# Performance work log

Measured on AMD Instinct MI355X. Metric: run time of the kernel, lower is better.

## Reference

```python
import jax, jax.numpy as jnp
import numpy as np

CODEBOOK_SIZE = 8192
DIM = 64
B, N = 4, 4096


def setup_inputs() -> dict:
    key = jax.random.key(0)
    k1, k2 = jax.random.split(key)
    x = jax.random.normal(k1, (B, N, DIM), dtype=jnp.float32)
    node_mask = jnp.ones((B, N), dtype=jnp.float32)
    embed = jax.random.normal(k2, (CODEBOOK_SIZE, DIM), dtype=jnp.float32)
    return {"x": x, "node_mask": node_mask, "embed": embed}


def reference(x, node_mask, embed):
    # x: [B, N, D]; embed: [K, D]; node_mask: [B, N]
    b, n, d = x.shape
    k = embed.shape[0]
    flatten = x.reshape(-1, d)  # [B*N, D]
    dist = -(
        jnp.sum(flatten * flatten, axis=1, keepdims=True)
        - 2.0 * (flatten @ embed.T)
        + jnp.sum(embed * embed, axis=1)[None, :]
    )
    embed_ind = jnp.argmax(dist, axis=-1)  # [B*N] nearest-code assignment
    quantize = embed[embed_ind].reshape(b, n, d)  # codebook gather
    # masked one-hot stats (embed_onehot * node_mask), via segment_sum
    mask_flat = node_mask.reshape(-1)
    counts = jax.ops.segment_sum(mask_flat, embed_ind, num_segments=k)  # [K]
    avg_probs = counts / jnp.asarray(flatten.shape[0], dtype=x.dtype)
    perplexity = jnp.exp(-jnp.sum(avg_probs * jnp.log(avg_probs + 1e-10)))
    return quantize, embed_ind.reshape(b, n), perplexity
```

## Files before the change

### kernel.cpp

```cpp
#include <hip/hip_runtime.h>

typedef __attribute__((ext_vector_type(8))) short short8;
typedef __attribute__((ext_vector_type(4))) float f32x4;

#define ROWS 16384
#define DIM 64
#define NCODES 8192
#define MARGIN 0.008f
#define KT_FB 256

#define WS_BEST   0
#define WS_COUNTS 131072
#define WS_ENH    163840
#define WS_ESWZ   196608
#define WS_NEED   2293760

__device__ __forceinline__ unsigned long long pack_score(float s, int idx) {
  unsigned u = __float_as_uint(s);
  u ^= (unsigned)((int)u >> 31) | 0x80000000u;
  return ((unsigned long long)u << 32) | (unsigned)(0xFFFF - idx);
}
__device__ __forceinline__ unsigned short bf16hi(float f) {
  unsigned u = __float_as_uint(f);
  return (unsigned short)((u + 0x7FFFu + ((u >> 16) & 1u)) >> 16);
}

__global__ void vq_enorm(const float* __restrict__ embed, float* __restrict__ enh) {
  int k = blockIdx.x * 256 + threadIdx.x;
  const float4* e4 = (const float4*)(embed + (size_t)k * DIM);
  float a = 0.f, b = 0.f, c = 0.f, d = 0.f;
#pragma unroll
  for (int i = 0; i < DIM / 4; ++i) {
    float4 v = e4[i];
    a = fmaf(v.x, v.x, a); b = fmaf(v.y, v.y, b);
    c = fmaf(v.z, v.z, c); d = fmaf(v.w, v.w, d);
  }
  enh[k] = 0.5f * ((a + b) + (c + d));
}

__global__ void vq_prep_e(const float* __restrict__ embed, short* __restrict__ eswz) {
  int u = blockIdx.x * 256 + threadIdx.x;
  int l = u & 63, kc = (u >> 6) & 1, ct = u >> 7;
  int code = ct * 16 + (l & 15);
  int kb = kc * 32 + (l >> 4) * 8;
  const float* er = embed + (size_t)code * DIM + kb;
  short8 h8, l8;
#pragma unroll
  for (int j = 0; j < 8; ++j) {
    float v = er[j];
    unsigned short h = bf16hi(v);
    float r = v - __uint_as_float((unsigned)h << 16);
    h8[j] = (short)h;
    l8[j] = (short)bf16hi(r);
  }
  short8* dst = (short8*)eswz;
  size_t frag = (size_t)(ct * 2 + kc) * 2;
  dst[(frag + 0) * 64 + l] = h8;
  dst[(frag + 1) * 64 + l] = l8;
}

__global__ __launch_bounds__(256, 2) void vq_screen(
    const float* __restrict__ x, const float* __restrict__ embed,
    const short* __restrict__ eswz, const float* __restrict__ enh,
    unsigned long long* __restrict__ best) {
  const int l = threadIdx.x & 63, wid = threadIdx.x >> 6;
  const int cl = l & 15, grp = l >> 4;
  const int row0 = blockIdx.x * 256 + wid * 64;
  const int ct0 = blockIdx.y * 64;

  short8 ahi[4][2], alo[4][2];
#pragma unroll
  for (int s = 0; s < 4; ++s) {
    const float* xr = x + (size_t)(row0 + s * 16 + cl) * DIM;
#pragma unroll
    for (int kc = 0; kc < 2; ++kc) {
      const int kb = kc * 32 + grp * 8;
#pragma unroll
      for (int j = 0; j < 8; ++j) {
        float v = xr[kb + j];
        unsigned short h = bf16hi(v);
        float r = v - __uint_as_float((unsigned)h << 16);
        ahi[s][kc][j] = (short)h;
        alo[s][kc][j] = (short)bf16hi(r);
      }
    }
  }

  const short8* eb = (const short8*)eswz;
  float bsc[4][4];
  int bidx[4][4];
#pragma unroll
  for (int s = 0; s < 4; ++s)
#pragma unroll
    for (int j = 0; j < 4; ++j) { bsc[s][j] = -3.4e38f; bidx[s][j] = 0; }

  short8 bh0, bl0, bh1, bl1;
  float eh;
  {
    size_t f0 = (size_t)(ct0 * 2 + 0) * 128, f1 = (size_t)(ct0 * 2 + 1) * 128;
    bh0 = eb[f0 + l]; bl0 = eb[f0 + 64 + l];
    bh1 = eb[f1 + l]; bl1 = eb[f1 + 64 + l];
    eh = enh[ct0 * 16 + cl];
  }

  for (int ct = ct0; ct < ct0 + 64; ++ct) {
    int ctn = (ct + 1 < ct0 + 64) ? ct + 1 : ct;
    size_t fn0 = (size_t)(ctn * 2 + 0) * 128, fn1 = (size_t)(ctn * 2 + 1) * 128;
    short8 nh0 = eb[fn0 + l], nl0 = eb[fn0 + 64 + l];
    short8 nh1 = eb[fn1 + l], nl1 = eb[fn1 + 64 + l];
    float ehx = enh[ctn * 16 + cl];

    f32x4 z = {0.f, 0.f, 0.f, 0.f};
    f32x4 acc0 = z, acc1 = z, acc2 = z, acc3 = z;
    acc0 = __builtin_amdgcn_mfma_f32_16x16x32_bf16(ahi[0][0], bh0, acc0, 0, 0, 0);
    acc1 = __builtin_amdgcn_mfma_f32_16x16x32_bf16(ahi[1][0], bh0, acc1, 0, 0, 0);
    acc2 = __builtin_amdgcn_mfma_f32_16x16x32_bf16(ahi[2][0], bh0, acc2, 0, 0, 0);
    acc3 = __builtin_amdgcn_mfma_f32_16x16x32_bf16(ahi[3][0], bh0, acc3, 0, 0, 0);
    acc0 = __builtin_amdgcn_mfma_f32_16x16x32_bf16(alo[0][0], bh0, acc0, 0, 0, 0);
    acc1 = __builtin_amdgcn_mfma_f32_16x16x32_bf16(alo[1][0], bh0, acc1, 0, 0, 0);
    acc2 = __builtin_amdgcn_mfma_f32_16x16x32_bf16(alo[2][0], bh0, acc2, 0, 0, 0);
    acc3 = __builtin_amdgcn_mfma_f32_16x16x32_bf16(alo[3][0], bh0, acc3, 0, 0, 0);
    acc0 = __builtin_amdgcn_mfma_f32_16x16x32_bf16(ahi[0][0], bl0, acc0, 0, 0, 0);
    acc1 = __builtin_amdgcn_mfma_f32_16x16x32_bf16(ahi[1][0], bl0, acc1, 0, 0, 0);
    acc2 = __builtin_amdgcn_mfma_f32_16x16x32_bf16(ahi[2][0], bl0, acc2, 0, 0, 0);
    acc3 = __builtin_amdgcn_mfma_f32_16x16x32_bf16(ahi[3][0], bl0, acc3, 0, 0, 0);
    acc0 = __builtin_amdgcn_mfma_f32_16x16x32_bf16(ahi[0][1], bh1, acc0, 0, 0, 0);
    acc1 = __builtin_amdgcn_mfma_f32_16x16x32_bf16(ahi[1][1], bh1, acc1, 0, 0, 0);
    acc2 = __builtin_amdgcn_mfma_f32_16x16x32_bf16(ahi[2][1], bh1, acc2, 0, 0, 0);
    acc3 = __builtin_amdgcn_mfma_f32_16x16x32_bf16(ahi[3][1], bh1, acc3, 0, 0, 0);
    acc0 = __builtin_amdgcn_mfma_f32_16x16x32_bf16(alo[0][1], bh1, acc0, 0, 0, 0);
    acc1 = __builtin_amdgcn_mfma_f32_16x16x32_bf16(alo[1][1], bh1, acc1, 0, 0, 0);
    acc2 = __builtin_amdgcn_mfma_f32_16x16x32_bf16(alo[2][1], bh1, acc2, 0, 0, 0);
    acc3 = __builtin_amdgcn_mfma_f32_16x16x32_bf16(alo[3][1], bh1, acc3, 0, 0, 0);
    acc0 = __builtin_amdgcn_mfma_f32_16x16x32_bf16(ahi[0][1], bl1, acc0, 0, 0, 0);
    acc1 = __builtin_amdgcn_mfma_f32_16x16x32_bf16(ahi[1][1], bl1, acc1, 0, 0, 0);
    acc2 = __builtin_amdgcn_mfma_f32_16x16x32_bf16(ahi[2][1], bl1, acc2, 0, 0, 0);
    acc3 = __builtin_amdgcn_mfma_f32_16x16x32_bf16(ahi[3][1], bl1, acc3, 0, 0, 0);

    const int code = ct * 16 + cl;
#pragma unroll
    for (int j = 0; j < 4; ++j) {
      float s0 = acc0[j] - eh, s1 = acc1[j] - eh, s2 = acc2[j] - eh, s3 = acc3[j] - eh;
      if (s0 > bsc[0][j]) { bsc[0][j] = s0; bidx[0][j] = code; }
      if (s1 > bsc[1][j]) { bsc[1][j] = s1; bidx[1][j] = code; }
      if (s2 > bsc[2][j]) { bsc[2][j] = s2; bidx[2][j] = code; }
      if (s3 > bsc[3][j]) { bsc[3][j] = s3; bidx[3][j] = code; }
    }
    bh0 = nh0; bl0 = nl0; bh1 = nh1; bl1 = nl1; eh = ehx;
  }

  unsigned fmask = 0;
#pragma unroll
  for (int s = 0; s < 4; ++s)
#pragma unroll
    for (int j = 0; j < 4; ++j) {
      float m = bsc[s][j];
      m = fmaxf(m, __shfl_xor(m, 1));
      m = fmaxf(m, __shfl_xor(m, 2));
      m = fmaxf(m, __shfl_xor(m, 4));
      m = fmaxf(m, __shfl_xor(m, 8));
      if (bsc[s][j] >= m - MARGIN) fmask |= 1u << (s * 4 + j);
    }

  float exact[4][4];
#pragma unroll
  for (int s = 0; s < 4; ++s)
#pragma unroll
    for (int j = 0; j < 4; ++j) exact[s][j] = -3.4e38f;

  while (__any((int)(fmask != 0))) {
    const bool act = fmask != 0;
    const int sel = __ffs(fmask) - 1;
    int code = 0;
#pragma unroll
    for (int s = 0; s < 4; ++s)
#pragma unroll
      for (int j = 0; j < 4; ++j)
        code = (sel == s * 4 + j) ? bidx[s][j] : code;
    int row = act ? (row0 + (sel >> 2) * 16 + grp * 4 + (sel & 3)) : row0;
    if (!act) code = 0;
    const float4* xr = (const float4*)(x + (size_t)row * DIM);
    const float4* er = (const float4*)(embed + (size_t)code * DIM);
    float a0 = 0, a1 = 0, a2 = 0, a3 = 0, n0 = 0, n1 = 0, n2 = 0, n3 = 0;
#pragma unroll
    for (int i = 0; i < 16; ++i) {
      float4 xv = xr[i], ev = er[i];
      a0 = fmaf(xv.x, ev.x, a0); a1 = fmaf(xv.y, ev.y, a1);
      a2 = fmaf(xv.z, ev.z, a2); a3 = fmaf(xv.w, ev.w, a3);
      n0 = fmaf(ev.x, ev.x, n0); n1 = fmaf(ev.y, ev.y, n1);
      n2 = fmaf(ev.z, ev.z, n2); n3 = fmaf(ev.w, ev.w, n3);
    }
    float ex = ((a0 + a1) + (a2 + a3)) - 0.5f * ((n0 + n1) + (n2 + n3));
#pragma unroll
    for (int s = 0; s < 4; ++s)
#pragma unroll
      for (int j = 0; j < 4; ++j)
        exact[s][j] = (act && sel == s * 4 + j) ? ex : exact[s][j];
    fmask = act ? (fmask & (fmask - 1)) : 0u;
  }

#pragma unroll
  for (int s = 0; s < 4; ++s)
#pragma unroll
    for (int j = 0; j < 4; ++j) {
      unsigned long long pk = pack_score(exact[s][j], bidx[s][j]);
      unsigned long long o;
      o = __shfl_xor(pk, 1); pk = pk > o ? pk : o;
      o = __shfl_xor(pk, 2); pk = pk > o ? pk : o;
      o = __shfl_xor(pk, 4); pk = pk > o ? pk : o;
      o = __shfl_xor(pk, 8); pk = pk > o ? pk : o;
      if (cl == 0) atomicMax(&best[row0 + s * 16 + grp * 4 + j], pk);
    }
}

__global__ __launch_bounds__(256, 2) void vq_score_fb(
    const float* __restrict__ x, const float* __restrict__ embed,
    const float* __restrict__ enh, unsigned long long* __restrict__ best) {
  const int row = blockIdx.x * 256 + threadIdx.x;
  const int c0 = blockIdx.y * KT_FB;
  float4 xa[16];
  const float4* xg = (const float4*)(x + (size_t)row * DIM);
#pragma unroll
  for (int i = 0; i < 16; ++i) xa[i] = xg[i];
  float bs = -3.4e38f;
  int bc = 0;
#pragma unroll 2
  for (int c = c0; c < c0 + KT_FB; ++c) {
    const float4* e4 = (const float4*)(embed + (size_t)c * DIM);
    float a0 = 0.f, a1 = 0.f, a2 = 0.f, a3 = 0.f;
#pragma unroll
    for (int i = 0; i < 16; ++i) {
      float4 ev = e4[i];
      a0 = fmaf(xa[i].x, ev.x, a0); a1 = fmaf(xa[i].y, ev.y, a1);
      a2 = fmaf(xa[i].z, ev.z, a2); a3 = fmaf(xa[i].w, ev.w, a3);
    }
    float s = ((a0 + a1) + (a2 + a3)) - enh[c];
    if (s > bs) { bs = s; bc = c; }
  }
  atomicMax(&best[row], pack_score(bs, bc));
}

__global__ void vq_finalize(const unsigned long long* __restrict__ best,
                            const float* __restrict__ embed,
                            const float* __restrict__ node_mask,
                            float* __restrict__ quant,
                            float* __restrict__ out_idx,
                            float* __restrict__ counts) {
  int gid = blockIdx.x * 256 + threadIdx.x;
  int row = gid >> 6, d = gid & 63;
  unsigned long long p = best[row];
  int idx = 0xFFFF - (int)(p & 0xFFFFull);
  quant[gid] = embed[(size_t)idx * DIM + d];
  if (d == 0) {
    out_idx[row] = (float)idx;
    atomicAdd(&counts[idx], node_mask[row]);
  }
}

__global__ void vq_perplexity(const float* __restrict__ counts, float* __restrict__ out) {
  int tid = threadIdx.x;
  float acc = 0.f;
  for (int k = tid; k < NCODES; k += 256) {
    float p = counts[k] * (1.0f / (float)ROWS);
    acc += p * logf(p + 1e-10f);
  }
#pragma unroll
  for (int off = 32; off > 0; off >>= 1) acc += __shfl_down(acc, off);
  __shared__ float red[4];
  if ((tid & 63) == 0) red[tid >> 6] = acc;
  __syncthreads();
  if (tid == 0) out[0] = expf(-((red[0] + red[1]) + (red[2] + red[3])));
}

extern "C" void kernel_launch(void* const* d_in, const int* in_sizes, int n_in,
                              void* d_out, int out_size, void* d_ws, size_t ws_size,
                              hipStream_t stream) {
  const float* x = (const float*)d_in[0];
  const float* node_mask = (const float*)d_in[1];
  const float* embed = (const float*)d_in[2];

  float* out = (float*)d_out;
  float* quant = out;
  float* out_idx = out + (size_t)ROWS * DIM;
  float* out_ppl = out_idx + ROWS;

  unsigned long long* best = (unsigned long long*)((char*)d_ws + WS_BEST);
  float* counts = (float*)((char*)d_ws + WS_COUNTS);
  float* enh = (float*)((char*)d_ws + WS_ENH);
  short* eswz = (short*)((char*)d_ws + WS_ESWZ);

  hipMemsetAsync(d_ws, 0, WS_ENH, stream);
  vq_enorm<<<NCODES / 256, 256, 0, stream>>>(embed, enh);
  if (ws_size >= WS_NEED) {
    vq_prep_e<<<256, 256, 0, stream>>>(embed, eswz);
    vq_screen<<<dim3(ROWS / 256, NCODES / 1024), 256, 0, stream>>>(x, embed, eswz, enh, best);
  } else {
    vq_score_fb<<<dim3(ROWS / 256, NCODES / KT_FB), 256, 0, stream>>>(x, embed, enh, best);
  }
  vq_finalize<<<ROWS * DIM / 256, 256, 0, stream>>>(best, embed, node_mask, quant, out_idx, counts);
  vq_perplexity<<<1, 256, 0, stream>>>(counts, out_ppl);
}
```

Before: 132.0 us.

## Halve code tiles per block, raise occupancy, fold norm into accumulator init

The screening kernel now handles 32 code tiles per block instead of 64, which doubles the grid along the codebook axis. Launch bounds go from 2 to 4 blocks per CU. The explicit software prefetch registers are replaced by a 2x unrolled loop. The negative code norm is used as the MFMA accumulator's initial value, so the per-element subtraction disappears. The aim is more occupancy and less register pressure to hide load latency, but it doubles the per-block epilogue and refinement work and may cause spills under the tighter register budget.

```diff
diff --git a/kernel.cpp b/kernel.cpp
--- a/kernel.cpp
+++ b/kernel.cpp
@@ -8,6 +8,7 @@
 #define NCODES 8192
 #define MARGIN 0.008f
 #define KT_FB 256
+#define CTS_PER_BLOCK 32
 
 #define WS_BEST   0
 #define WS_COUNTS 131072
@@ -59,14 +60,14 @@
   dst[(frag + 1) * 64 + l] = l8;
 }
 
-__global__ __launch_bounds__(256, 2) void vq_screen(
+__global__ __launch_bounds__(256, 4) void vq_screen(
     const float* __restrict__ x, const float* __restrict__ embed,
     const short* __restrict__ eswz, const float* __restrict__ enh,
     unsigned long long* __restrict__ best) {
   const int l = threadIdx.x & 63, wid = threadIdx.x >> 6;
   const int cl = l & 15, grp = l >> 4;
   const int row0 = blockIdx.x * 256 + wid * 64;
-  const int ct0 = blockIdx.y * 64;
+  const int ct0 = blockIdx.y * CTS_PER_BLOCK;
 
   short8 ahi[4][2], alo[4][2];
 #pragma unroll
@@ -94,24 +95,15 @@
 #pragma unroll
     for (int j = 0; j < 4; ++j) { bsc[s][j] = -3.4e38f; bidx[s][j] = 0; }
 
-  short8 bh0, bl0, bh1, bl1;
-  float eh;
-  {
-    size_t f0 = (size_t)(ct0 * 2 + 0) * 128, f1 = (size_t)(ct0 * 2 + 1) * 128;
-    bh0 = eb[f0 + l]; bl0 = eb[f0 + 64 + l];
-    bh1 = eb[f1 + l]; bl1 = eb[f1 + 64 + l];
-    eh = enh[ct0 * 16 + cl];
-  }
-
-  for (int ct = ct0; ct < ct0 + 64; ++ct) {
-    int ctn = (ct + 1 < ct0 + 64) ? ct + 1 : ct;
-    size_t fn0 = (size_t)(ctn * 2 + 0) * 128, fn1 = (size_t)(ctn * 2 + 1) * 128;
-    short8 nh0 = eb[fn0 + l], nl0 = eb[fn0 + 64 + l];
-    short8 nh1 = eb[fn1 + l], nl1 = eb[fn1 + 64 + l];
-    float ehx = enh[ctn * 16 + cl];
-
-    f32x4 z = {0.f, 0.f, 0.f, 0.f};
-    f32x4 acc0 = z, acc1 = z, acc2 = z, acc3 = z;
+#pragma unroll 2
+  for (int ct = ct0; ct < ct0 + CTS_PER_BLOCK; ++ct) {
+    size_t f0 = (size_t)(ct * 2 + 0) * 128, f1 = (size_t)(ct * 2 + 1) * 128;
+    short8 bh0 = eb[f0 + l], bl0 = eb[f0 + 64 + l];
+    short8 bh1 = eb[f1 + l], bl1 = eb[f1 + 64 + l];
+    float eh = enh[ct * 16 + cl];
+
+    f32x4 accI = {-eh, -eh, -eh, -eh};
+    f32x4 acc0 = accI, acc1 = accI, acc2 = accI, acc3 = accI;
     acc0 = __builtin_amdgcn_mfma_f32_16x16x32_bf16(ahi[0][0], bh0, acc0, 0, 0, 0);
     acc1 = __builtin_amdgcn_mfma_f32_16x16x32_bf16(ahi[1][0], bh0, acc1, 0, 0, 0);
     acc2 = __builtin_amdgcn_mfma_f32_16x16x32_bf16(ahi[2][0], bh0, acc2, 0, 0, 0);
@@ -140,13 +132,11 @@
     const int code = ct * 16 + cl;
 #pragma unroll
     for (int j = 0; j < 4; ++j) {
-      float s0 = acc0[j] - eh, s1 = acc1[j] - eh, s2 = acc2[j] - eh, s3 = acc3[j] - eh;
-      if (s0 > bsc[0][j]) { bsc[0][j] = s0; bidx[0][j] = code; }
-      if (s1 > bsc[1][j]) { bsc[1][j] = s1; bidx[1][j] = code; }
-      if (s2 > bsc[2][j]) { bsc[2][j] = s2; bidx[2][j] = code; }
-      if (s3 > bsc[3][j]) { bsc[3][j] = s3; bidx[3][j] = code; }
-    }
-    bh0 = nh0; bl0 = nl0; bh1 = nh1; bl1 = nl1; eh = ehx;
+      if (acc0[j] > bsc[0][j]) { bsc[0][j] = acc0[j]; bidx[0][j] = code; }
+      if (acc1[j] > bsc[1][j]) { bsc[1][j] = acc1[j]; bidx[1][j] = code; }
+      if (acc2[j] > bsc[2][j]) { bsc[2][j] = acc2[j]; bidx[2][j] = code; }
+      if (acc3[j] > bsc[3][j]) { bsc[3][j] = acc3[j]; bidx[3][j] = code; }
+    }
   }
 
   unsigned fmask = 0;
@@ -293,7 +283,8 @@
   vq_enorm<<<NCODES / 256, 256, 0, stream>>>(embed, enh);
   if (ws_size >= WS_NEED) {
     vq_prep_e<<<256, 256, 0, stream>>>(embed, eswz);
-    vq_screen<<<dim3(ROWS / 256, NCODES / 1024), 256, 0, stream>>>(x, embed, eswz, enh, best);
+    vq_screen<<<dim3(ROWS / 256, NCODES / (CTS_PER_BLOCK * 16)), 256, 0, stream>>>(
+        x, embed, eswz, enh, best);
   } else {
     vq_score_fb<<<dim3(ROWS / 256, NCODES / KT_FB), 256, 0, stream>>>(x, embed, enh, best);
   }
```

Result: slower. 160.3 us (+21.4%).
